# Performance work log

Hardware: AMD Instinct MI355X
Metric: run time of the kernel (lower is better)

The kernel has to match this reference:

```python
import math
import jax, jax.numpy as jnp
import numpy as np

S, B, H = 2048, 1, 4096
NH, HD = 32, 128          # heads, head dim
ROT = HD // 2             # rotary dim per 2D-RoPE half = 64


def rotate_half(x):
    x1, x2 = jnp.split(x, 2, axis=-1)
    return jnp.concatenate([-x2, x1], axis=-1)


def rope_tables(seq_len, dim, base=10000.0):
    inv_freq = 1.0 / (base ** (jnp.arange(0, dim, 2, dtype=jnp.float32) / dim))
    freqs = jnp.arange(seq_len, dtype=jnp.float32)[:, None] * inv_freq[None, :]
    emb = jnp.concatenate([freqs, freqs], axis=-1)  # [S, dim]
    return jnp.cos(emb), jnp.sin(emb)


def apply_rope(q, k, cos, sin, pos):
    # q,k: [S,B,NH,ROT]; pos: [S,B] -> gather cos/sin per token
    c = cos[pos][:, :, None, :]  # [S,B,1,ROT]
    s = sin[pos][:, :, None, :]
    return q * c + rotate_half(q) * s, k * c + rotate_half(k) * s


def setup_inputs() -> dict:
    key = jax.random.key(0)
    ks = jax.random.split(key, 5)
    hidden_states = jax.random.normal(ks[0], (S, B, H), dtype=jnp.float32)
    pos = jnp.arange(S, dtype=jnp.int64 if jax.config.jax_enable_x64 else jnp.int32)
    position_ids = jnp.stack([pos, pos])[None]  # [B=1, 2, S]
    attention_mask = jnp.triu(jnp.ones((S, S), dtype=bool), k=1)[None, None]  # True = masked
    scale = 0.02
    wqkv = jax.random.normal(ks[1], (3 * H, H), dtype=jnp.float32) * scale
    bqkv = jax.random.normal(ks[2], (3 * H,), dtype=jnp.float32) * scale
    wdense = jax.random.normal(ks[3], (H, H), dtype=jnp.float32) * scale
    bdense = jax.random.normal(ks[4], (H,), dtype=jnp.float32) * scale
    return {"hidden_states": hidden_states, "position_ids": position_ids,
            "attention_mask": attention_mask, "wqkv": wqkv, "bqkv": bqkv,
            "wdense": wdense, "bdense": bdense, "layer_id": 1}


def reference(hidden_states, position_ids, attention_mask, wqkv, bqkv, wdense, bdense, layer_id):
    s, b, h = hidden_states.shape
    # fused QKV projection: [S,B,NH,3*HD]
    mixed = (jnp.einsum('sbh,oh->sbo', hidden_states, wqkv) + bqkv).reshape(s, b, NH, 3 * HD)
    q, k, v = jnp.split(mixed, 3, axis=-1)  # each [S,B,NH,HD]

    # 2D RoPE: split head dim in half, rotate each half with its own position ids
    q1, q2 = jnp.split(q, 2, axis=-1)
    k1, k2 = jnp.split(k, 2, axis=-1)
    cos, sin = rope_tables(s, ROT)
    pos = position_ids[:, 0, :].T       # [S,B]
    block_pos = position_ids[:, 1, :].T  # [S,B]
    q1, k1 = apply_rope(q1, k1, cos, sin, pos)
    q2, k2 = apply_rope(q2, k2, cos, sin, block_pos)
    q = jnp.concatenate([q1, q2], axis=-1)
    k = jnp.concatenate([k1, k2], axis=-1)

    # layer-scaled attention (ChatGLM style)
    coeff = float(layer_id + 1)
    q = q / (math.sqrt(HD) * coeff)
    scores = jnp.einsum('sbhd,tbhd->bhst', q, k)  # [B,NH,S,S]
    scores = jnp.where(attention_mask, jnp.float32(-10000.0), scores)
    scores = scores.astype(jnp.float32) * coeff
    probs = jax.nn.softmax(scores, axis=-1).astype(q.dtype)
    context = jnp.einsum('bhst,tbhd->sbhd', probs, v).reshape(s, b, h)

    out = jnp.einsum('sbh,oh->sbo', context, wdense) + bdense
    return out
```

## Files before the change

kernel.cpp:

```cpp
#include <hip/hip_runtime.h>

typedef unsigned short u16;
typedef unsigned int u32;
typedef __attribute__((ext_vector_type(4))) float f32x4;
typedef __attribute__((ext_vector_type(8))) short bf16x8;
typedef __attribute__((ext_vector_type(2))) unsigned int u32x2;

#define S_LEN 2048
#define NHEAD 32
#define HDD 128
#define HID 4096
#define N_QKV 12288
#define KDIM 4096
#define RS 12288

__device__ __forceinline__ u16 f2bf(float f) {
  u32 u = __builtin_bit_cast(u32, f);
  u = (u + 0x7FFFu + ((u >> 16) & 1u)) >> 16;
  return (u16)u;
}
__device__ __forceinline__ float bf2f(u16 h) {
  u32 u = ((u32)h) << 16;
  return __builtin_bit_cast(float, u);
}

__device__ __forceinline__ void gl2lds16(const void* g, void* l) {
  __builtin_amdgcn_global_load_lds(
      (const __attribute__((address_space(1))) u32*)g,
      (__attribute__((address_space(3))) u32*)l, 16, 0, 0);
}

#define FULL_BAR()                          \
  {                                         \
    asm volatile("" ::: "memory");          \
    __builtin_amdgcn_s_barrier();           \
    asm volatile("" ::: "memory");          \
  }

__global__ __launch_bounds__(256) void cvt3_kernel(const float* __restrict__ s0, u16* __restrict__ d0, int n0,
                                                   const float* __restrict__ s1, u16* __restrict__ d1, int n1,
                                                   const float* __restrict__ s2, u16* __restrict__ d2, int n2) {
  int i = blockIdx.x * blockDim.x + threadIdx.x;
  int st = gridDim.x * blockDim.x;
  int ntot = n0 + n1 + n2;
  for (; i < ntot; i += st) {
    const float* s;
    u16* d;
    int j = i;
    if (j < n0) {
      s = s0; d = d0;
    } else if (j < n0 + n1) {
      j -= n0; s = s1; d = d1;
    } else {
      j -= n0 + n1; s = s2; d = d2;
    }
    float4 v = ((const float4*)s)[j];
    u32x2 o;
    o.x = (u32)f2bf(v.x) | ((u32)f2bf(v.y) << 16);
    o.y = (u32)f2bf(v.z) | ((u32)f2bf(v.w) << 16);
    ((u32x2*)d)[j] = o;
  }
}

__global__ __launch_bounds__(256) void tables_kernel(float* __restrict__ cos_t,
                                                     float* __restrict__ sin_t) {
  int idx = blockIdx.x * blockDim.x + threadIdx.x;
  if (idx >= S_LEN * 32) return;
  int s = idx >> 5, i = idx & 31;
  float invf = expf(-0.28782313662425572f * (float)i);
  float a = (float)s * invf;
  cos_t[idx] = cosf(a);
  sin_t[idx] = sinf(a);
}

__global__ __launch_bounds__(256) void rope_kernel(u16* __restrict__ mixed,
                                                   const int* __restrict__ pid,
                                                   const float* __restrict__ cos_t,
                                                   const float* __restrict__ sin_t) {
  int idx = blockIdx.x * blockDim.x + threadIdx.x;
  const int total = 2 * NHEAD * S_LEN * 2 * 8;
  if (idx >= total) return;
  int j = idx & 7;
  int half = (idx >> 3) & 1;
  int s = (idx >> 4) & (S_LEN - 1);
  int h = (idx >> 15) & (NHEAD - 1);
  int qk = idx >> 20;
  int i0 = j * 4;
  int p = pid[half * S_LEN + s];
  float4 c4 = *(const float4*)(cos_t + p * 32 + i0);
  float4 s4 = *(const float4*)(sin_t + p * 32 + i0);
  u16* base = mixed + (size_t)s * RS + h * 384 + qk * 128 + half * 64 + i0;
  ushort4 x1v = *(const ushort4*)(base);
  ushort4 x2v = *(const ushort4*)(base + 32);
  float sc = qk ? 1.0f : 0.08838834764831845f;
  ushort4 o1, o2;
  {
    float x1 = bf2f(x1v.x), x2 = bf2f(x2v.x);
    o1.x = f2bf((x1 * c4.x - x2 * s4.x) * sc);
    o2.x = f2bf((x2 * c4.x + x1 * s4.x) * sc);
  }
  {
    float x1 = bf2f(x1v.y), x2 = bf2f(x2v.y);
    o1.y = f2bf((x1 * c4.y - x2 * s4.y) * sc);
    o2.y = f2bf((x2 * c4.y + x1 * s4.y) * sc);
  }
  {
    float x1 = bf2f(x1v.z), x2 = bf2f(x2v.z);
    o1.z = f2bf((x1 * c4.z - x2 * s4.z) * sc);
    o2.z = f2bf((x2 * c4.z + x1 * s4.z) * sc);
  }
  {
    float x1 = bf2f(x1v.w), x2 = bf2f(x2v.w);
    o1.w = f2bf((x1 * c4.w - x2 * s4.w) * sc);
    o2.w = f2bf((x2 * c4.w + x1 * s4.w) * sc);
  }
  *(ushort4*)(base) = o1;
  *(ushort4*)(base + 32) = o2;
}

template <int NI, int EPI>
__global__ __launch_bounds__(512, 2) void gemmK(const u16* __restrict__ A,
                                                const u16* __restrict__ B,
                                                const float* __restrict__ bias, int N, int NTt,
                                                u16* __restrict__ outb, float* __restrict__ outf) {
  constexpr int BN = NI * 64;
  constexpr int BSUB = NI * 4096;
  constexpr int BUFSZ = 32768 + 2 * BSUB;
  __shared__ __align__(16) char lds[2][BUFSZ];

  const int tid = threadIdx.x;
  const int lane = tid & 63, w = tid >> 6;
  const int l15 = lane & 15, g = lane >> 4;
  const int wm = w >> 2, wn = w & 3;

  int perx = gridDim.x >> 3;
  int npx = perx >> 3;
  int x = blockIdx.x & 7, loc = blockIdx.x >> 3;
  int mb = loc & 7, nb = x * npx + (loc >> 3);
  const int bm = mb * 256, bn = nb * BN;

  const u16* Ag = A + (size_t)blockIdx.y * 2048;
  const u16* Bg = B + (size_t)blockIdx.y * 2048;

  f32x4 acc[8][NI];
  f32x4 z4 = {0.f, 0.f, 0.f, 0.f};
#pragma unroll
  for (int mi = 0; mi < 8; ++mi)
#pragma unroll
    for (int ni = 0; ni < NI; ++ni) acc[mi][ni] = z4;

  const size_t K2 = (size_t)KDIM * 2;

  const char* gA[2];
#pragma unroll
  for (int j = 0; j < 2; ++j) {
    int slot = j * 512 + tid;
    int line = slot >> 3;
    int sl = (slot & 7) ^ (line & 7);
    int row = 2 * line + (sl >> 2);
    int colb = (sl & 3) * 16;
    gA[j] = (const char*)Ag + (size_t)(bm + row) * K2 + colb;
  }
  const char* gB[NI];
#pragma unroll
  for (int j = 0; j < NI; ++j) {
    int n_ = j * 512 + tid;
    int kkj = (n_ >= NI * 256) ? 1 : 0;
    int m_ = n_ - kkj * NI * 256;
    int line = m_ >> 3;
    int sl = (m_ & 7) ^ (line & 7);
    int row = 2 * line + (sl >> 2);
    int colb = (sl & 3) * 16;
    gB[j] = (const char*)Bg + (size_t)(bn + row) * K2 + kkj * 64 + colb;
  }
  const int ldst = w * 1024;

#define ISSUE_A(t, kk)                                                        \
  {                                                                           \
    char* Lb = lds[(t) & 1] + (kk) * 16384;                                   \
    gl2lds16(gA[0] + (size_t)(t) * 128 + (kk) * 64, Lb + ldst);               \
    gl2lds16(gA[1] + (size_t)(t) * 128 + (kk) * 64, Lb + 8192 + ldst);        \
  }
#define ISSUE_B(t)                                                            \
  {                                                                           \
    char* Lb = lds[(t) & 1] + 32768;                                          \
    _Pragma("unroll")                                                         \
    for (int j = 0; j < NI; ++j)                                              \
      gl2lds16(gB[j] + (size_t)(t) * 128, Lb + j * 8192 + ldst);              \
  }

  int offA[8], offB[2][NI];
#pragma unroll
  for (int mi = 0; mi < 8; ++mi) {
    int r = wm * 128 + mi * 16 + l15;
    int line = r >> 1;
    int sl = (((r & 1) << 2) + g) ^ (line & 7);
    offA[mi] = line * 128 + sl * 16;
  }
#pragma unroll
  for (int kk = 0; kk < 2; ++kk)
#pragma unroll
    for (int ni = 0; ni < NI; ++ni) {
      int r = wn * (NI * 16) + ni * 16 + l15;
      int line = r >> 1;
      int sl = (((r & 1) << 2) + g) ^ (line & 7);
      offB[kk][ni] = 32768 + kk * BSUB + line * 128 + sl * 16;
    }

  ISSUE_A(0, 0);
  ISSUE_B(0);
  ISSUE_A(0, 1);
  asm volatile("s_waitcnt vmcnt(0)" ::: "memory");
  FULL_BAR();

  for (int kt = 0; kt < NTt; ++kt) {
    const char* buf = lds[kt & 1];
    const bool pf = (kt + 1) < NTt;
    bf16x8 a[4], b[NI];
#pragma unroll
    for (int mi = 0; mi < 4; ++mi) a[mi] = *(const bf16x8*)(buf + offA[mi]);
#pragma unroll
    for (int ni = 0; ni < NI; ++ni) b[ni] = *(const bf16x8*)(buf + offB[0][ni]);
    if (pf) ISSUE_A(kt + 1, 0);
    FULL_BAR();
    __builtin_amdgcn_s_setprio(1);
#pragma unroll
    for (int mi = 0; mi < 4; ++mi)
#pragma unroll
      for (int ni = 0; ni < NI; ++ni)
        acc[mi][ni] = __builtin_amdgcn_mfma_f32_16x16x32_bf16(a[mi], b[ni], acc[mi][ni], 0, 0, 0);
    __builtin_amdgcn_s_setprio(0);
#pragma unroll
    for (int mi = 0; mi < 4; ++mi) a[mi] = *(const bf16x8*)(buf + offA[4 + mi]);
    if (pf) ISSUE_B(kt + 1);
    if (pf) {
      if constexpr (NI == 3) {
        asm volatile("s_waitcnt vmcnt(5)" ::: "memory");
      } else {
        asm volatile("s_waitcnt vmcnt(6)" ::: "memory");
      }
    } else {
      asm volatile("s_waitcnt vmcnt(0)" ::: "memory");
    }
    FULL_BAR();
    __builtin_amdgcn_s_setprio(1);
#pragma unroll
    for (int mi = 0; mi < 4; ++mi)
#pragma unroll
      for (int ni = 0; ni < NI; ++ni)
        acc[4 + mi][ni] = __builtin_amdgcn_mfma_f32_16x16x32_bf16(a[mi], b[ni], acc[4 + mi][ni], 0, 0, 0);
    __builtin_amdgcn_s_setprio(0);
#pragma unroll
    for (int mi = 0; mi < 4; ++mi) a[mi] = *(const bf16x8*)(buf + 16384 + offA[mi]);
#pragma unroll
    for (int ni = 0; ni < NI; ++ni) b[ni] = *(const bf16x8*)(buf + offB[1][ni]);
    if (pf) ISSUE_A(kt + 1, 1);
    FULL_BAR();
    __builtin_amdgcn_s_setprio(1);
#pragma unroll
    for (int mi = 0; mi < 4; ++mi)
#pragma unroll
      for (int ni = 0; ni < NI; ++ni)
        acc[mi][ni] = __builtin_amdgcn_mfma_f32_16x16x32_bf16(a[mi], b[ni], acc[mi][ni], 0, 0, 0);
    __builtin_amdgcn_s_setprio(0);
#pragma unroll
    for (int mi = 0; mi < 4; ++mi) a[mi] = *(const bf16x8*)(buf + 16384 + offA[4 + mi]);
    if (pf) asm volatile("s_waitcnt vmcnt(2)" ::: "memory");
    FULL_BAR();
    __builtin_amdgcn_s_setprio(1);
#pragma unroll
    for (int mi = 0; mi < 4; ++mi)
#pragma unroll
      for (int ni = 0; ni < NI; ++ni)
        acc[4 + mi][ni] = __builtin_amdgcn_mfma_f32_16x16x32_bf16(a[mi], b[ni], acc[4 + mi][ni], 0, 0, 0);
    __builtin_amdgcn_s_setprio(0);
  }
#undef ISSUE_A
#undef ISSUE_B

  float* of = outf ? outf + (size_t)blockIdx.y * S_LEN * N : nullptr;
#pragma unroll
  for (int ni = 0; ni < NI; ++ni) {
    int n = bn + wn * (NI * 16) + ni * 16 + l15;
    if (EPI == 0) {
      float bv = bias[n];
#pragma unroll
      for (int mi = 0; mi < 8; ++mi) {
        int m0 = bm + wm * 128 + mi * 16 + 4 * g;
#pragma unroll
        for (int rr = 0; rr < 4; ++rr)
          outb[(size_t)(m0 + rr) * N + n] = f2bf(acc[mi][ni][rr] + bv);
      }
    } else {
#pragma unroll
      for (int mi = 0; mi < 8; ++mi) {
        int m0 = bm + wm * 128 + mi * 16 + 4 * g;
#pragma unroll
        for (int rr = 0; rr < 4; ++rr) of[(size_t)(m0 + rr) * N + n] = acc[mi][ni][rr];
      }
    }
  }
}

__global__ __launch_bounds__(256) void reduce_kernel(const float* __restrict__ P0,
                                                     const float* __restrict__ P1,
                                                     const float* __restrict__ bias,
                                                     float* __restrict__ out, int n4) {
  int i = blockIdx.x * blockDim.x + threadIdx.x;
  int st = gridDim.x * blockDim.x;
  for (; i < n4; i += st) {
    float4 a = ((const float4*)P0)[i];
    float4 b = ((const float4*)P1)[i];
    float4 bv = *(const float4*)(bias + ((i * 4) & (HID - 1)));
    float4 o;
    o.x = a.x + b.x + bv.x;
    o.y = a.y + b.y + bv.y;
    o.z = a.z + b.z + bv.z;
    o.w = a.w + b.w + bv.w;
    ((float4*)out)[i] = o;
  }
}

__global__ __launch_bounds__(256) void attn_kernel(const u16* __restrict__ mixed,
                                                   u16* __restrict__ ctx) {
  __shared__ __align__(16) u16 Ksh[32 * 136];
  __shared__ __align__(16) u16 Vsh[128 * 32];
  __shared__ __align__(16) u16 Pt[4][16 * 40];

  int tid = threadIdx.x;
  int lane = tid & 63, w = tid >> 6;
  int lane15 = lane & 15, g = lane >> 4;
  int h = blockIdx.y;
  int qbase = blockIdx.x * 64;
  int qrow = qbase + w * 16 + lane15;

  const u16* qp = mixed + (size_t)h * 384;
  const u16* kp = mixed + (size_t)h * 384 + 128;
  const u16* vp = mixed + (size_t)h * 384 + 256;

  bf16x8 qf[4];
  const u16* qptr = qp + (size_t)qrow * RS + g * 8;
#pragma unroll
  for (int d0 = 0; d0 < 4; ++d0) qf[d0] = *(const bf16x8*)(qptr + d0 * 32);

  f32x4 pv[8];
  f32x4 z4 = {0.f, 0.f, 0.f, 0.f};
#pragma unroll
  for (int db = 0; db < 8; ++db) pv[db] = z4;
  float m_run = -1e30f, l_run = 0.0f;

  int krow = tid >> 3, kc = (tid & 7) * 16;
  int a_ = tid & 15, b_ = tid >> 4;
  int ntiles = (qbase >> 5) + 2;

  for (int t = 0; t < ntiles; ++t) {
    int kb0 = t * 32;
    __syncthreads();
    {
      const bf16x8* src = (const bf16x8*)(kp + (size_t)(kb0 + krow) * RS + kc);
      bf16x8 x0 = src[0], x1 = src[1];
      *(bf16x8*)(Ksh + krow * 136 + kc) = x0;
      *(bf16x8*)(Ksh + krow * 136 + kc + 8) = x1;
      int k0 = 2 * a_, d0 = 8 * b_;
      bf16x8 r0 = *(const bf16x8*)(vp + (size_t)(kb0 + k0) * RS + d0);
      bf16x8 r1 = *(const bf16x8*)(vp + (size_t)(kb0 + k0 + 1) * RS + d0);
#pragma unroll
      for (int jj = 0; jj < 8; ++jj) {
        int d = d0 + jj;
        u32 val = (u32)(u16)r0[jj] | ((u32)(u16)r1[jj] << 16);
        *(u32*)(Vsh + d * 32 + (((k0 >> 3) ^ (d & 3)) << 3) + (k0 & 7)) = val;
      }
    }
    __syncthreads();

    f32x4 sa0 = z4, sa1 = z4;
#pragma unroll
    for (int d0 = 0; d0 < 4; ++d0) {
      bf16x8 k0f = *(const bf16x8*)(Ksh + lane15 * 136 + d0 * 32 + g * 8);
      bf16x8 k1f = *(const bf16x8*)(Ksh + (16 + lane15) * 136 + d0 * 32 + g * 8);
      sa0 = __builtin_amdgcn_mfma_f32_16x16x32_bf16(k0f, qf[d0], sa0, 0, 0, 0);
      sa1 = __builtin_amdgcn_mfma_f32_16x16x32_bf16(k1f, qf[d0], sa1, 0, 0, 0);
    }
    float s[8];
#pragma unroll
    for (int rr = 0; rr < 4; ++rr) {
      int kg0 = kb0 + 4 * g + rr;
      int kg1 = kb0 + 16 + 4 * g + rr;
      s[rr] = (kg0 > qrow) ? -1e30f : sa0[rr];
      s[4 + rr] = (kg1 > qrow) ? -1e30f : sa1[rr];
    }
    float mx = s[0];
#pragma unroll
    for (int i = 1; i < 8; ++i) mx = fmaxf(mx, s[i]);
    mx = fmaxf(mx, __shfl_xor(mx, 16));
    mx = fmaxf(mx, __shfl_xor(mx, 32));
    float mnew = fmaxf(m_run, mx);
    float fac = exp2f((m_run - mnew) * 1.4426950408889634f);
    float p[8], psum = 0.f;
#pragma unroll
    for (int i = 0; i < 8; ++i) {
      p[i] = exp2f((s[i] - mnew) * 1.4426950408889634f);
      psum += p[i];
    }
    psum += __shfl_xor(psum, 16);
    psum += __shfl_xor(psum, 32);
    l_run = l_run * fac + psum;
    m_run = mnew;
#pragma unroll
    for (int db = 0; db < 8; ++db) pv[db] *= fac;

    u32 w0 = (u32)f2bf(p[0]) | ((u32)f2bf(p[1]) << 16);
    u32 w1 = (u32)f2bf(p[2]) | ((u32)f2bf(p[3]) << 16);
    u32 w2 = (u32)f2bf(p[4]) | ((u32)f2bf(p[5]) << 16);
    u32 w3 = (u32)f2bf(p[6]) | ((u32)f2bf(p[7]) << 16);
    u32x2 pa, pb;
    pa.x = w0; pa.y = w1; pb.x = w2; pb.y = w3;
    *(u32x2*)(&Pt[w][lane15 * 40 + 4 * g]) = pa;
    *(u32x2*)(&Pt[w][lane15 * 40 + 16 + 4 * g]) = pb;
    asm volatile("s_waitcnt lgkmcnt(0)" ::: "memory");
    bf16x8 pfrag = *(const bf16x8*)(&Pt[w][lane15 * 40 + 8 * g]);

#pragma unroll
    for (int db = 0; db < 8; ++db) {
      int d = db * 16 + lane15;
      bf16x8 vf = *(const bf16x8*)(Vsh + d * 32 + ((g ^ (d & 3)) << 3));
      pv[db] = __builtin_amdgcn_mfma_f32_16x16x32_bf16(vf, pfrag, pv[db], 0, 0, 0);
    }
  }

  float inv = 1.0f / l_run;
#pragma unroll
  for (int db = 0; db < 8; ++db) {
    ushort4 o;
    o.x = f2bf(pv[db][0] * inv);
    o.y = f2bf(pv[db][1] * inv);
    o.z = f2bf(pv[db][2] * inv);
    o.w = f2bf(pv[db][3] * inv);
    *(ushort4*)(ctx + (size_t)qrow * HID + h * HDD + db * 16 + 4 * g) = o;
  }
}

extern "C" void kernel_launch(void* const* d_in, const int* in_sizes, int n_in,
                              void* d_out, int out_size, void* d_ws, size_t ws_size,
                              hipStream_t stream) {
  const float* hidden = (const float*)d_in[0];
  const int* pid = (const int*)d_in[1];
  const float* wqkv = (const float*)d_in[3];
  const float* bqkv = (const float*)d_in[4];
  const float* wdense = (const float*)d_in[5];
  const float* bdense = (const float*)d_in[6];
  float* out = (float*)d_out;

  char* ws = (char*)d_ws;
  u16* W1 = (u16*)ws;
  u16* W2 = (u16*)(ws + 100663296);
  u16* X = (u16*)(ws + 134217728);
  u16* mixed = (u16*)(ws + 150994944);
  u16* ctx = (u16*)(ws + 201326592);
  float* cos_t = (float*)(ws + 218103808);
  float* sin_t = (float*)(ws + 218365952);
  float* P = (float*)ws;

  cvt3_kernel<<<dim3(2048), dim3(256), 0, stream>>>(
      wqkv, W1, N_QKV * KDIM / 4, wdense, W2, HID * KDIM / 4, hidden, X, S_LEN * HID / 4);
  tables_kernel<<<dim3(256), dim3(256), 0, stream>>>(cos_t, sin_t);

  gemmK<3, 0><<<dim3(512), dim3(512), 0, stream>>>(
      X, W1, bqkv, N_QKV, 64, mixed, nullptr);

  rope_kernel<<<dim3(8192), dim3(256), 0, stream>>>(mixed, pid, cos_t, sin_t);

  attn_kernel<<<dim3(S_LEN / 64, NHEAD), dim3(256), 0, stream>>>(mixed, ctx);

  gemmK<4, 1><<<dim3(128, 2), dim3(512), 0, stream>>>(
      ctx, W2, nullptr, HID, 32, nullptr, P);

  reduce_kernel<<<dim3(2048), dim3(256), 0, stream>>>(
      P, P + (size_t)S_LEN * HID, bdense, out, S_LEN * HID / 4);
}
```

Measured before the change: 540.5 us.

## Rework GEMM warp tiling, drop split-K dense GEMM, balance causal attention blocks

The GEMM kernel changes its warp layout from 2x4 warps with 8 M-fragments to 4x2 warps with 4 M-fragments and NW N-fragments. The QKV GEMM now uses a 192-wide N tile and the dense GEMM a 128-wide tile. The output GEMM no longer splits K across two partial buffers; it runs full K with the bias fused into its epilogue, which removes the reduce kernel and the partial-sum traffic. Attention blocks are launched in a 1D order that pairs short and long causal query blocks so that load is spread more evenly across the GPU. Accumulator register counts and per-block work change, which may affect occupancy and the dense GEMM's parallelism.

```diff
diff --git a/kernel.cpp b/kernel.cpp
--- a/kernel.cpp
+++ b/kernel.cpp
@@ -118,20 +118,22 @@
   *(ushort4*)(base + 32) = o2;
 }
 
-template <int NI, int EPI>
+template <int NW, int EPI>
 __global__ __launch_bounds__(512, 2) void gemmK(const u16* __restrict__ A,
                                                 const u16* __restrict__ B,
                                                 const float* __restrict__ bias, int N, int NTt,
                                                 u16* __restrict__ outb, float* __restrict__ outf) {
-  constexpr int BN = NI * 64;
-  constexpr int BSUB = NI * 4096;
+  constexpr int BN = 32 * NW;
+  constexpr int NLB = NW / 2;
+  constexpr int BSUB = BN * 64;
   constexpr int BUFSZ = 32768 + 2 * BSUB;
+  constexpr int NH2 = NW / 2;
   __shared__ __align__(16) char lds[2][BUFSZ];
 
   const int tid = threadIdx.x;
   const int lane = tid & 63, w = tid >> 6;
   const int l15 = lane & 15, g = lane >> 4;
-  const int wm = w >> 2, wn = w & 3;
+  const int wm = w >> 1, wn = w & 1;
 
   int perx = gridDim.x >> 3;
   int npx = perx >> 3;
@@ -139,15 +141,12 @@
   int mb = loc & 7, nb = x * npx + (loc >> 3);
   const int bm = mb * 256, bn = nb * BN;
 
-  const u16* Ag = A + (size_t)blockIdx.y * 2048;
-  const u16* Bg = B + (size_t)blockIdx.y * 2048;
-
-  f32x4 acc[8][NI];
+  f32x4 acc[4][NW];
   f32x4 z4 = {0.f, 0.f, 0.f, 0.f};
 #pragma unroll
-  for (int mi = 0; mi < 8; ++mi)
-#pragma unroll
-    for (int ni = 0; ni < NI; ++ni) acc[mi][ni] = z4;
+  for (int mi = 0; mi < 4; ++mi)
+#pragma unroll
+    for (int ni = 0; ni < NW; ++ni) acc[mi][ni] = z4;
 
   const size_t K2 = (size_t)KDIM * 2;
 
@@ -159,19 +158,19 @@
     int sl = (slot & 7) ^ (line & 7);
     int row = 2 * line + (sl >> 2);
     int colb = (sl & 3) * 16;
-    gA[j] = (const char*)Ag + (size_t)(bm + row) * K2 + colb;
-  }
-  const char* gB[NI];
-#pragma unroll
-  for (int j = 0; j < NI; ++j) {
+    gA[j] = (const char*)A + (size_t)(bm + row) * K2 + colb;
+  }
+  const char* gB[NLB];
+#pragma unroll
+  for (int j = 0; j < NLB; ++j) {
     int n_ = j * 512 + tid;
-    int kkj = (n_ >= NI * 256) ? 1 : 0;
-    int m_ = n_ - kkj * NI * 256;
+    int kkj = (n_ >= 128 * NW) ? 1 : 0;
+    int m_ = n_ - kkj * 128 * NW;
     int line = m_ >> 3;
     int sl = (m_ & 7) ^ (line & 7);
     int row = 2 * line + (sl >> 2);
     int colb = (sl & 3) * 16;
-    gB[j] = (const char*)Bg + (size_t)(bn + row) * K2 + kkj * 64 + colb;
+    gB[j] = (const char*)B + (size_t)(bn + row) * K2 + kkj * 64 + colb;
   }
   const int ldst = w * 1024;
 
@@ -185,14 +184,14 @@
   {                                                                           \
     char* Lb = lds[(t) & 1] + 32768;                                          \
     _Pragma("unroll")                                                         \
-    for (int j = 0; j < NI; ++j)                                              \
+    for (int j = 0; j < NLB; ++j)                                             \
       gl2lds16(gB[j] + (size_t)(t) * 128, Lb + j * 8192 + ldst);              \
   }
 
-  int offA[8], offB[2][NI];
-#pragma unroll
-  for (int mi = 0; mi < 8; ++mi) {
-    int r = wm * 128 + mi * 16 + l15;
+  int offA[4], offB[2][NW];
+#pragma unroll
+  for (int mi = 0; mi < 4; ++mi) {
+    int r = wm * 64 + mi * 16 + l15;
     int line = r >> 1;
     int sl = (((r & 1) << 2) + g) ^ (line & 7);
     offA[mi] = line * 128 + sl * 16;
@@ -200,8 +199,8 @@
 #pragma unroll
   for (int kk = 0; kk < 2; ++kk)
 #pragma unroll
-    for (int ni = 0; ni < NI; ++ni) {
-      int r = wn * (NI * 16) + ni * 16 + l15;
+    for (int ni = 0; ni < NW; ++ni) {
+      int r = wn * (16 * NW) + ni * 16 + l15;
       int line = r >> 1;
       int sl = (((r & 1) << 2) + g) ^ (line & 7);
       offB[kk][ni] = 32768 + kk * BSUB + line * 128 + sl * 16;
@@ -216,29 +215,25 @@
   for (int kt = 0; kt < NTt; ++kt) {
     const char* buf = lds[kt & 1];
     const bool pf = (kt + 1) < NTt;
-    bf16x8 a[4], b[NI];
+    bf16x8 a[4], b[NH2];
 #pragma unroll
     for (int mi = 0; mi < 4; ++mi) a[mi] = *(const bf16x8*)(buf + offA[mi]);
 #pragma unroll
-    for (int ni = 0; ni < NI; ++ni) b[ni] = *(const bf16x8*)(buf + offB[0][ni]);
+    for (int ni = 0; ni < NH2; ++ni) b[ni] = *(const bf16x8*)(buf + offB[0][ni]);
     if (pf) ISSUE_A(kt + 1, 0);
     FULL_BAR();
     __builtin_amdgcn_s_setprio(1);
 #pragma unroll
     for (int mi = 0; mi < 4; ++mi)
 #pragma unroll
-      for (int ni = 0; ni < NI; ++ni)
+      for (int ni = 0; ni < NH2; ++ni)
         acc[mi][ni] = __builtin_amdgcn_mfma_f32_16x16x32_bf16(a[mi], b[ni], acc[mi][ni], 0, 0, 0);
     __builtin_amdgcn_s_setprio(0);
 #pragma unroll
-    for (int mi = 0; mi < 4; ++mi) a[mi] = *(const bf16x8*)(buf + offA[4 + mi]);
+    for (int ni = 0; ni < NH2; ++ni) b[ni] = *(const bf16x8*)(buf + offB[0][NH2 + ni]);
     if (pf) ISSUE_B(kt + 1);
     if (pf) {
-      if constexpr (NI == 3) {
-        asm volatile("s_waitcnt vmcnt(5)" ::: "memory");
-      } else {
-        asm volatile("s_waitcnt vmcnt(6)" ::: "memory");
-      }
+      asm volatile("s_waitcnt vmcnt(%0)" ::"i"(2 + NLB) : "memory");
     } else {
       asm volatile("s_waitcnt vmcnt(0)" ::: "memory");
     }
@@ -247,77 +242,57 @@
 #pragma unroll
     for (int mi = 0; mi < 4; ++mi)
 #pragma unroll
-      for (int ni = 0; ni < NI; ++ni)
-        acc[4 + mi][ni] = __builtin_amdgcn_mfma_f32_16x16x32_bf16(a[mi], b[ni], acc[4 + mi][ni], 0, 0, 0);
+      for (int ni = 0; ni < NH2; ++ni)
+        acc[mi][NH2 + ni] = __builtin_amdgcn_mfma_f32_16x16x32_bf16(a[mi], b[ni], acc[mi][NH2 + ni], 0, 0, 0);
     __builtin_amdgcn_s_setprio(0);
 #pragma unroll
     for (int mi = 0; mi < 4; ++mi) a[mi] = *(const bf16x8*)(buf + 16384 + offA[mi]);
 #pragma unroll
-    for (int ni = 0; ni < NI; ++ni) b[ni] = *(const bf16x8*)(buf + offB[1][ni]);
+    for (int ni = 0; ni < NH2; ++ni) b[ni] = *(const bf16x8*)(buf + offB[1][ni]);
     if (pf) ISSUE_A(kt + 1, 1);
     FULL_BAR();
     __builtin_amdgcn_s_setprio(1);
 #pragma unroll
     for (int mi = 0; mi < 4; ++mi)
 #pragma unroll
-      for (int ni = 0; ni < NI; ++ni)
+      for (int ni = 0; ni < NH2; ++ni)
         acc[mi][ni] = __builtin_amdgcn_mfma_f32_16x16x32_bf16(a[mi], b[ni], acc[mi][ni], 0, 0, 0);
     __builtin_amdgcn_s_setprio(0);
 #pragma unroll
-    for (int mi = 0; mi < 4; ++mi) a[mi] = *(const bf16x8*)(buf + 16384 + offA[4 + mi]);
+    for (int ni = 0; ni < NH2; ++ni) b[ni] = *(const bf16x8*)(buf + offB[1][NH2 + ni]);
     if (pf) asm volatile("s_waitcnt vmcnt(2)" ::: "memory");
     FULL_BAR();
     __builtin_amdgcn_s_setprio(1);
 #pragma unroll
     for (int mi = 0; mi < 4; ++mi)
 #pragma unroll
-      for (int ni = 0; ni < NI; ++ni)
-        acc[4 + mi][ni] = __builtin_amdgcn_mfma_f32_16x16x32_bf16(a[mi], b[ni], acc[4 + mi][ni], 0, 0, 0);
+      for (int ni = 0; ni < NH2; ++ni)
+        acc[mi][NH2 + ni] = __builtin_amdgcn_mfma_f32_16x16x32_bf16(a[mi], b[ni], acc[mi][NH2 + ni], 0, 0, 0);
     __builtin_amdgcn_s_setprio(0);
   }
 #undef ISSUE_A
 #undef ISSUE_B
 
-  float* of = outf ? outf + (size_t)blockIdx.y * S_LEN * N : nullptr;
-#pragma unroll
-  for (int ni = 0; ni < NI; ++ni) {
-    int n = bn + wn * (NI * 16) + ni * 16 + l15;
+#pragma unroll
+  for (int ni = 0; ni < NW; ++ni) {
+    int n = bn + wn * (16 * NW) + ni * 16 + l15;
+    float bv = bias[n];
     if (EPI == 0) {
-      float bv = bias[n];
-#pragma unroll
-      for (int mi = 0; mi < 8; ++mi) {
-        int m0 = bm + wm * 128 + mi * 16 + 4 * g;
+#pragma unroll
+      for (int mi = 0; mi < 4; ++mi) {
+        int m0 = bm + wm * 64 + mi * 16 + 4 * g;
 #pragma unroll
         for (int rr = 0; rr < 4; ++rr)
           outb[(size_t)(m0 + rr) * N + n] = f2bf(acc[mi][ni][rr] + bv);
       }
     } else {
 #pragma unroll
-      for (int mi = 0; mi < 8; ++mi) {
-        int m0 = bm + wm * 128 + mi * 16 + 4 * g;
-#pragma unroll
-        for (int rr = 0; rr < 4; ++rr) of[(size_t)(m0 + rr) * N + n] = acc[mi][ni][rr];
+      for (int mi = 0; mi < 4; ++mi) {
+        int m0 = bm + wm * 64 + mi * 16 + 4 * g;
+#pragma unroll
+        for (int rr = 0; rr < 4; ++rr) outf[(size_t)(m0 + rr) * N + n] = acc[mi][ni][rr] + bv;
       }
     }
-  }
-}
-
-__global__ __launch_bounds__(256) void reduce_kernel(const float* __restrict__ P0,
-                                                     const float* __restrict__ P1,
-                                                     const float* __restrict__ bias,
-                                                     float* __restrict__ out, int n4) {
-  int i = blockIdx.x * blockDim.x + threadIdx.x;
-  int st = gridDim.x * blockDim.x;
-  for (; i < n4; i += st) {
-    float4 a = ((const float4*)P0)[i];
-    float4 b = ((const float4*)P1)[i];
-    float4 bv = *(const float4*)(bias + ((i * 4) & (HID - 1)));
-    float4 o;
-    o.x = a.x + b.x + bv.x;
-    o.y = a.y + b.y + bv.y;
-    o.z = a.z + b.z + bv.z;
-    o.w = a.w + b.w + bv.w;
-    ((float4*)out)[i] = o;
   }
 }
 
@@ -330,8 +305,16 @@
   int tid = threadIdx.x;
   int lane = tid & 63, w = tid >> 6;
   int lane15 = lane & 15, g = lane >> 4;
-  int h = blockIdx.y;
-  int qbase = blockIdx.x * 64;
+
+  int i = blockIdx.x;
+  int qb_base = i & 7;
+  int h = (i >> 3) & 31;
+  int quarter = i >> 8;
+  int qbi = (quarter == 0) ? qb_base
+            : (quarter == 1) ? (15 - qb_base)
+            : (quarter == 2) ? (16 + qb_base)
+                             : (31 - qb_base);
+  int qbase = qbi * 64;
   int qrow = qbase + w * 16 + lane15;
 
   const u16* qp = mixed + (size_t)h * 384;
@@ -391,16 +374,16 @@
     }
     float mx = s[0];
 #pragma unroll
-    for (int i = 1; i < 8; ++i) mx = fmaxf(mx, s[i]);
+    for (int i2 = 1; i2 < 8; ++i2) mx = fmaxf(mx, s[i2]);
     mx = fmaxf(mx, __shfl_xor(mx, 16));
     mx = fmaxf(mx, __shfl_xor(mx, 32));
     float mnew = fmaxf(m_run, mx);
     float fac = exp2f((m_run - mnew) * 1.4426950408889634f);
     float p[8], psum = 0.f;
 #pragma unroll
-    for (int i = 0; i < 8; ++i) {
-      p[i] = exp2f((s[i] - mnew) * 1.4426950408889634f);
-      psum += p[i];
+    for (int i2 = 0; i2 < 8; ++i2) {
+      p[i2] = exp2f((s[i2] - mnew) * 1.4426950408889634f);
+      psum += p[i2];
     }
     psum += __shfl_xor(psum, 16);
     psum += __shfl_xor(psum, 32);
@@ -459,22 +442,18 @@
   u16* ctx = (u16*)(ws + 201326592);
   float* cos_t = (float*)(ws + 218103808);
   float* sin_t = (float*)(ws + 218365952);
-  float* P = (float*)ws;
 
   cvt3_kernel<<<dim3(2048), dim3(256), 0, stream>>>(
       wqkv, W1, N_QKV * KDIM / 4, wdense, W2, HID * KDIM / 4, hidden, X, S_LEN * HID / 4);
   tables_kernel<<<dim3(256), dim3(256), 0, stream>>>(cos_t, sin_t);
 
-  gemmK<3, 0><<<dim3(512), dim3(512), 0, stream>>>(
+  gemmK<6, 0><<<dim3(512), dim3(512), 0, stream>>>(
       X, W1, bqkv, N_QKV, 64, mixed, nullptr);
 
   rope_kernel<<<dim3(8192), dim3(256), 0, stream>>>(mixed, pid, cos_t, sin_t);
 
-  attn_kernel<<<dim3(S_LEN / 64, NHEAD), dim3(256), 0, stream>>>(mixed, ctx);
-
-  gemmK<4, 1><<<dim3(128, 2), dim3(512), 0, stream>>>(
-      ctx, W2, nullptr, HID, 32, nullptr, P);
-
-  reduce_kernel<<<dim3(2048), dim3(256), 0, stream>>>(
-      P, P + (size_t)S_LEN * HID, bdense, out, S_LEN * HID / 4);
-}
+  attn_kernel<<<dim3(1024), dim3(256), 0, stream>>>(mixed, ctx);
+
+  gemmK<4, 1><<<dim3(256), dim3(512), 0, stream>>>(
+      ctx, W2, bdense, HID, 64, nullptr, out);
+}
```

Measured after the change: 497.8 us. 1.09x faster.
